# Kernel tuning notes

Hardware: AMD Instinct MI355X
Metric: run time of the kernel (lower is better)

Reference implementation:

```python
import jax, jax.numpy as jnp
import numpy as np

FEAT = 256
NUM_ATOMS = np.array([2048, 1536, 1024, 2048, 512, 1792, 1280, 2048], dtype=np.int32)
B = len(NUM_ATOMS)
N = int(NUM_ATOMS.sum())          # 12288 total atoms
MAXN = int(NUM_ATOMS.max())       # 2048
# Static segment bookkeeping (num_atoms is structural, not data)
_OFFSETS = np.concatenate([[0], np.cumsum(NUM_ATOMS)[:-1]])
SEG = np.repeat(np.arange(B), NUM_ATOMS)            # [N] graph id per atom
POS = np.arange(N) - _OFFSETS[SEG]                  # [N] position within graph
VALID = np.arange(MAXN)[None, :] < NUM_ATOMS[:, None]  # [B, MAXN] key mask


def setup_inputs() -> dict:
    key = jax.random.key(0)
    k1, k2 = jax.random.split(key)
    s = jax.random.normal(k1, (N, FEAT), jnp.float32)
    # dense: feat_dim -> 3*feat_dim, with bias
    W = jax.random.normal(k2, (FEAT, 3 * FEAT), jnp.float32) / np.float32(np.sqrt(FEAT))
    b = jnp.zeros((3 * FEAT,), jnp.float32)
    num_atoms = jnp.asarray(NUM_ATOMS)
    return {"s": s, "W": W, "b": b, "num_atoms": num_atoms}


def _pad(X):
    # scatter flat [N, FEAT] atoms into padded [B, MAXN, FEAT]
    return jnp.zeros((B, MAXN, FEAT), X.dtype).at[SEG, POS].set(X)


def reference(s, W, b, num_atoms):
    qkv = s @ W + b                          # [N, 3*FEAT]
    Q, K, V = jnp.split(qkv, 3, axis=-1)     # each [N, FEAT]
    Qp, Kp, Vp = _pad(Q), _pad(K), _pad(V)   # [B, MAXN, FEAT]
    scale = np.float32(1.0 / np.sqrt(FEAT))
    scores = jnp.einsum('bqd,bkd->bqk', Qp, Kp) * scale   # [B, MAXN, MAXN]
    scores = jnp.where(VALID[:, None, :], scores, -jnp.inf)  # mask padded keys
    att = jax.nn.softmax(scores, axis=-1)
    out = jnp.einsum('bqk,bkd->bqd', att, Vp)             # [B, MAXN, FEAT]
    return out[SEG, POS]                                   # back to flat [N, FEAT]
```

## Files before the change

kernel.cpp:

```cpp
#include <hip/hip_runtime.h>

typedef __attribute__((ext_vector_type(8))) short short8;
typedef __attribute__((ext_vector_type(4))) short s16x4;
typedef __attribute__((ext_vector_type(4))) float f32x4;

#define MFMA16(a,b,c) __builtin_amdgcn_mfma_f32_16x16x32_bf16((a),(b),(c),0,0,0)

__device__ __forceinline__ ushort f2bf(float f){ union{float f; unsigned u;} v; v.f=f; unsigned r=v.u + 0x7fffu + ((v.u>>16)&1u); return (ushort)(r>>16); }
__device__ __forceinline__ float bf2f(ushort u){ union{unsigned u; float f;} v; v.u = ((unsigned)u)<<16; return v.f; }

__global__ void __launch_bounds__(256) prep(const float* __restrict__ S,
    ushort* __restrict__ Sb, const float* __restrict__ W, ushort* __restrict__ Wt)
{
    __shared__ __align__(16) ushort tile[64*72];
    const int t = threadIdx.x;
    if (blockIdx.x < 1024){
        const int tid = blockIdx.x*256 + t;
#pragma unroll
        for (int r=0;r<3;r++){
            const int idx = tid + r*262144;
            f32x4 v = ((const f32x4*)S)[idx];
            s16x4 o;
            o[0]=(short)f2bf(v[0]); o[1]=(short)f2bf(v[1]);
            o[2]=(short)f2bf(v[2]); o[3]=(short)f2bf(v[3]);
            ((s16x4*)Sb)[idx] = o;
        }
    } else {
        const int i = blockIdx.x - 1024;
        const int r0 = (i&3)*64, c0 = (i>>2)*64;
        const int rr = t>>2, g = (t&3)*16;
        const float* sp = W + (size_t)(r0+rr)*768 + c0 + g;
#pragma unroll
        for (int j=0;j<16;j++) tile[(g+j)*72 + rr] = f2bf(sp[j]);
        __syncthreads();
        ushort* dp = Wt + (size_t)(c0+rr)*256 + r0 + g;
        *(short8*)dp     = *(const short8*)&tile[rr*72 + g];
        *(short8*)(dp+8) = *(const short8*)&tile[rr*72 + g + 8];
    }
}

__global__ void __launch_bounds__(256) qkv_gemm(const ushort* __restrict__ Sb,
    const ushort* __restrict__ Wt, const float* __restrict__ bias,
    ushort* __restrict__ Q, ushort* __restrict__ K, ushort* __restrict__ Vt)
{
    __shared__ __align__(16) ushort Bl[64*264];
    const int t = threadIdx.x, w = t>>6, l = t&63, lr = l&15, lq = l>>4;
    const int m0 = blockIdx.x*128, n0 = blockIdx.y*64;

    const ushort* ap = Sb + (size_t)(m0 + w*32 + lr)*256 + lq*8;
    short8 sa[2][8];
#pragma unroll
    for (int g=0;g<2;g++)
#pragma unroll
        for (int kc=0;kc<8;kc++)
            sa[g][kc] = *(const short8*)(ap + g*16*256 + kc*32);

#pragma unroll
    for (int s=0;s<8;s++){
        const int u = t + s*256, row = u>>5, c8 = u&31;
        *(short8*)&Bl[row*264 + c8*8] = *(const short8*)(Wt + (size_t)(n0+row)*256 + c8*8);
    }
    __syncthreads();

    if (n0 < 512){
        f32x4 acc[2][4];
#pragma unroll
        for (int a=0;a<2;a++)
#pragma unroll
            for (int b2=0;b2<4;b2++) acc[a][b2]=(f32x4){0.f,0.f,0.f,0.f};
#pragma unroll
        for (int kc=0;kc<8;kc++){
#pragma unroll
            for (int nt=0;nt<4;nt++){
                short8 bf = *(const short8*)&Bl[(nt*16+lr)*264 + lq*8 + kc*32];
                acc[0][nt] = MFMA16(sa[0][kc], bf, acc[0][nt]);
                acc[1][nt] = MFMA16(sa[1][kc], bf, acc[1][nt]);
            }
        }
        ushort* dst = (n0 < 256) ? Q : K;
        const int colbase = n0 & 255;
#pragma unroll
        for (int nt=0;nt<4;nt++){
            float bv = bias[n0 + nt*16 + lr];
#pragma unroll
            for (int mt=0;mt<2;mt++){
                const int row = m0 + w*32 + mt*16 + lq*4;
                ushort* o = dst + (size_t)row*256 + colbase + nt*16 + lr;
#pragma unroll
                for (int i=0;i<4;i++) o[(size_t)i*256] = f2bf(acc[mt][nt][i] + bv);
            }
        }
    } else {
        const int f0 = n0 - 512;
        f32x4 acc[4][2];
#pragma unroll
        for (int a=0;a<4;a++)
#pragma unroll
            for (int b2=0;b2<2;b2++) acc[a][b2]=(f32x4){0.f,0.f,0.f,0.f};
#pragma unroll
        for (int kc=0;kc<8;kc++){
#pragma unroll
            for (int ft=0;ft<4;ft++){
                short8 af = *(const short8*)&Bl[(ft*16+lr)*264 + lq*8 + kc*32];
                acc[ft][0] = MFMA16(af, sa[0][kc], acc[ft][0]);
                acc[ft][1] = MFMA16(af, sa[1][kc], acc[ft][1]);
            }
        }
#pragma unroll
        for (int ft=0;ft<4;ft++){
#pragma unroll
            for (int at=0;at<2;at++){
                ushort* o = Vt + (size_t)(f0 + ft*16 + lq*4)*12288 + m0 + w*32 + at*16 + lr;
#pragma unroll
                for (int i=0;i<4;i++){
                    float bv = bias[512 + f0 + ft*16 + lq*4 + i];
                    o[(size_t)i*12288] = f2bf(acc[ft][at][i] + bv);
                }
            }
        }
    }
}

template<int MODE>
__global__ void __launch_bounds__(256,2) attn_partial(const ushort* __restrict__ Qb,
    const ushort* __restrict__ Kb, const ushort* __restrict__ Vt,
    void* __restrict__ Optr, float* __restrict__ Lptr)
{
    __shared__ __align__(16) ushort Kl[32*264];
    __shared__ __align__(16) ushort Vl[256*40];
    const int t = threadIdx.x, w = t>>6, l = t&63, lr = l&15, lq = l>>4;

    const int offs[9] = {0,2048,3584,4608,6656,7168,8960,10240,12288};
    int bi = blockIdx.x, q0=0, kstart=0, kend=0, off=0, nbg=0, pbase=0, pb=0;
#pragma unroll
    for (int s=0;s<8;s++){
        const int nb = offs[s+1]-offs[s];
        const int tiles = nb>>7, pieces = (nb+511)>>9;
        const int items = tiles*pieces;
        if (bi >= 0 && bi < items){
            const int tile = bi / pieces, piece = bi - tile*pieces;
            q0 = offs[s] + tile*128;
            kstart = offs[s] + piece*512;
            kend = min(offs[s]+nb, kstart+512);
            off = offs[s]; nbg = nb; pbase = pb;
        }
        bi -= items;
        pb += nb*pieces;
    }
    const int nchunks = (kend - kstart) >> 5;
    const int pc = (kstart - off) >> 9;

    short8 qf[2][8];
#pragma unroll
    for (int g=0;g<2;g++){
        const ushort* qp = Qb + (size_t)(q0 + w*32 + g*16 + lr)*256 + lq*8;
#pragma unroll
        for (int kc=0;kc<8;kc++) qf[g][kc] = *(const short8*)(qp + kc*32);
    }
    f32x4 Oa[2][16];
#pragma unroll
    for (int g=0;g<2;g++)
#pragma unroll
        for (int ft=0;ft<16;ft++) Oa[g][ft] = (f32x4){0.f,0.f,0.f,0.f};
    float l_lane[2] = {0.f, 0.f};

    const int kr = t>>5, kcol = t&31;
    const ushort* kg0 = Kb + (size_t)(kstart + kr)*256 + kcol*8;
    const ushort* vg0 = Vt + (size_t)t*12288 + kstart;
    short8 kreg[4], vreg[4];
#pragma unroll
    for (int s=0;s<4;s++){
        kreg[s] = *(const short8*)(kg0 + (size_t)s*8*256);
        vreg[s] = *(const short8*)(vg0 + s*8);
    }

    const int i0 = 4*(lr + 32*(lq&1));
    const int i1 = i0 + 64;
    const bool hi = (lq >= 2);

    for (int ck=0; ck<nchunks; ck++){
#pragma unroll
        for (int s=0;s<4;s++)
            *(short8*)&Kl[(kr + s*8)*264 + kcol*8] = kreg[s];
#pragma unroll
        for (int s=0;s<4;s++)
            *(short8*)&Vl[t*40 + s*8] = vreg[s];
        if (ck+1 < nchunks){
            const ushort* kg = kg0 + (size_t)(ck+1)*32*256;
            const ushort* vg = vg0 + (ck+1)*32;
#pragma unroll
            for (int s=0;s<4;s++){
                kreg[s] = *(const short8*)(kg + (size_t)s*8*256);
                vreg[s] = *(const short8*)(vg + s*8);
            }
        }
        __syncthreads();

        f32x4 sc[2][2];
#pragma unroll
        for (int h=0;h<2;h++)
#pragma unroll
            for (int g=0;g<2;g++) sc[h][g] = (f32x4){0.f,0.f,0.f,0.f};
#pragma unroll
        for (int kc=0;kc<8;kc++){
            short8 b0 = *(const short8*)&Kl[ lr     *264 + kc*32 + lq*8];
            short8 b1 = *(const short8*)&Kl[(16+lr)*264 + kc*32 + lq*8];
#pragma unroll
            for (int g=0;g<2;g++){
                sc[0][g] = MFMA16(b0, qf[g][kc], sc[0][g]);
                sc[1][g] = MFMA16(b1, qf[g][kc], sc[1][g]);
            }
        }

        short8 pa[2];
#pragma unroll
        for (int g=0;g<2;g++){
            float p[8];
#pragma unroll
            for (int h=0;h<2;h++)
#pragma unroll
                for (int i=0;i<4;i++){
                    float v = exp2f(sc[h][g][i]*0.0901684284f);
                    p[h*4+i] = v;
                    l_lane[g] += v;
                }
            unsigned w0 = (unsigned)f2bf(p[0]) | ((unsigned)f2bf(p[1])<<16);
            unsigned w1 = (unsigned)f2bf(p[2]) | ((unsigned)f2bf(p[3])<<16);
            unsigned w2 = (unsigned)f2bf(p[4]) | ((unsigned)f2bf(p[5])<<16);
            unsigned w3 = (unsigned)f2bf(p[6]) | ((unsigned)f2bf(p[7])<<16);
            unsigned a0 = (unsigned)__builtin_amdgcn_ds_bpermute(i0, (int)w0);
            unsigned a2 = (unsigned)__builtin_amdgcn_ds_bpermute(i0, (int)w2);
            unsigned b1w= (unsigned)__builtin_amdgcn_ds_bpermute(i0, (int)w1);
            unsigned b3 = (unsigned)__builtin_amdgcn_ds_bpermute(i0, (int)w3);
            unsigned c0 = (unsigned)__builtin_amdgcn_ds_bpermute(i1, (int)w0);
            unsigned c2 = (unsigned)__builtin_amdgcn_ds_bpermute(i1, (int)w2);
            unsigned d1 = (unsigned)__builtin_amdgcn_ds_bpermute(i1, (int)w1);
            unsigned d3 = (unsigned)__builtin_amdgcn_ds_bpermute(i1, (int)w3);
            union { unsigned u[4]; short8 s8; } pk;
            pk.u[0] = hi ? a2 : a0;
            pk.u[1] = hi ? b3 : b1w;
            pk.u[2] = hi ? c2 : c0;
            pk.u[3] = hi ? d3 : d1;
            pa[g] = pk.s8;
        }

#pragma unroll
        for (int ft=0;ft<16;ft++){
            short8 vf = *(const short8*)&Vl[(ft*16+lr)*40 + lq*8];
            Oa[0][ft] = MFMA16(pa[0], vf, Oa[0][ft]);
            Oa[1][ft] = MFMA16(pa[1], vf, Oa[1][ft]);
        }
        __syncthreads();
    }

#pragma unroll
    for (int g=0;g<2;g++){
        float r = l_lane[g];
        r += __shfl_xor(r,16); r += __shfl_xor(r,32);
        l_lane[g] = r;
    }

    if constexpr (MODE == 0){
        ushort* Op = (ushort*)Optr;
        const int prow0 = pbase + pc*nbg + (q0 + w*32 - off);
#pragma unroll
        for (int g=0;g<2;g++)
#pragma unroll
            for (int i=0;i<4;i++){
                ushort* o = Op + (size_t)(prow0 + g*16 + lq*4 + i)*256 + lr;
#pragma unroll
                for (int ft=0;ft<16;ft++) o[ft*16] = f2bf(Oa[g][ft][i]);
            }
        if (l < 16){
            Lptr[prow0 + lr]      = l_lane[0];
            Lptr[prow0 + 16 + lr] = l_lane[1];
        }
    } else {
        float* out = (float*)Optr;
#pragma unroll
        for (int g=0;g<2;g++){
            float* op = out + (size_t)(q0 + w*32 + g*16 + lq*4)*256 + lr;
#pragma unroll
            for (int i=0;i<4;i++)
#pragma unroll
                for (int ft=0;ft<16;ft++)
                    atomicAdd(&op[(size_t)i*256 + ft*16], Oa[g][ft][i]);
        }
        if (l < 16){
            atomicAdd(&Lptr[q0 + w*32 + lr],      l_lane[0]);
            atomicAdd(&Lptr[q0 + w*32 + 16 + lr], l_lane[1]);
        }
    }
}

__global__ void __launch_bounds__(256) reduce_norm(const ushort* __restrict__ Opart,
    const float* __restrict__ Lpart, float* __restrict__ out, int PL)
{
    const int offs[9] = {0,2048,3584,4608,6656,7168,8960,10240,12288};
    const int t = threadIdx.x;
    const int row = blockIdx.x*8 + (t>>5);
    const int f = (t&31)*8;
    const int PIECE = 1 << PL;
    int pb = 0, nb = 0, S = 0, base = 0;
#pragma unroll
    for (int i=0;i<8;i++){
        const int nbi = offs[i+1]-offs[i];
        const int pieces = (nbi + PIECE-1) >> PL;
        if (row >= offs[i] && row < offs[i+1]){
            nb = nbi; S = pieces; base = pb + (row - offs[i]);
        }
        pb += nbi*pieces;
    }
    float acc[8] = {0.f,0.f,0.f,0.f,0.f,0.f,0.f,0.f};
    float L = 0.f;
    for (int p=0; p<S; p++){
        const size_t pr = (size_t)(base + p*nb);
        L += Lpart[pr];
        short8 v = *(const short8*)&Opart[pr*256 + f];
#pragma unroll
        for (int j=0;j<8;j++) acc[j] += bf2f((ushort)v[j]);
    }
    const float inv = 1.0f / L;
    f32x4 o0, o1;
#pragma unroll
    for (int j=0;j<4;j++){ o0[j] = acc[j]*inv; o1[j] = acc[4+j]*inv; }
    float* op = out + (size_t)row*256 + f;
    *(f32x4*)op     = o0;
    *(f32x4*)(op+4) = o1;
}

__global__ void __launch_bounds__(256) normalize_out(float* __restrict__ out,
    const float* __restrict__ lsum)
{
    const int row = blockIdx.x, t = threadIdx.x;
    const float inv = 1.0f / lsum[row];
    out[(size_t)row*256 + t] *= inv;
}

extern "C" void kernel_launch(void* const* d_in, const int* in_sizes, int n_in,
                              void* d_out, int out_size, void* d_ws, size_t ws_size,
                              hipStream_t stream)
{
    const float* S    = nullptr;
    const float* W    = nullptr;
    const float* bias = nullptr;
    for (int i = 0; i < n_in; i++){
        if      (in_sizes[i] == 3145728) S    = (const float*)d_in[i];
        else if (in_sizes[i] ==  196608) W    = (const float*)d_in[i];
        else if (in_sizes[i] ==     768) bias = (const float*)d_in[i];
    }
    if (!S)    S    = (const float*)d_in[0];
    if (!W)    W    = (const float*)d_in[1];
    if (!bias) bias = (const float*)d_in[2];

    float* out = (float*)d_out;

    ushort* ws  = (ushort*)d_ws;
    ushort* Wt  = ws;
    ushort* Qb  = Wt + 768*256;
    ushort* Kb  = Qb + 12288*256;
    ushort* Vtb = Kb + 12288*256;

    const size_t base_b  = ((size_t)768*256 + 3*(size_t)12288*256) * 2;
    const size_t need512 = base_b + (size_t)42752*512 + (size_t)42752*4;

    ushort* Sb = (ushort*)d_out;

    prep     <<<1072,        256, 0, stream>>>(S, Sb, W, Wt);
    qkv_gemm <<<dim3(96,12), 256, 0, stream>>>(Sb, Wt, bias, Qb, Kb, Vtb);

    if (ws_size >= need512){
        ushort* Opart = (ushort*)((char*)d_ws + base_b);
        float*  Lpart = (float*)((char*)d_ws + base_b + (size_t)42752*512);
        attn_partial<0><<<334, 256, 0, stream>>>(Qb, Kb, Vtb, (void*)Opart, Lpart);
        reduce_norm    <<<1536, 256, 0, stream>>>(Opart, Lpart, out, 9);
    } else {
        float* lsum = (float*)((char*)d_ws + base_b);
        (void)hipMemsetAsync(d_out, 0, (size_t)12288*256*4, stream);
        (void)hipMemsetAsync(lsum,  0, (size_t)12288*4,     stream);
        attn_partial<1><<<334, 256, 0, stream>>>(Qb, Kb, Vtb, (void*)out, lsum);
        normalize_out  <<<12288, 256, 0, stream>>>(out, lsum);
    }
}
```

Baseline: 158.7 us.

## Block the V-transpose layout per 32-key chunk and transpose PV MFMA output

Stores the transposed V as contiguous 32-key blocks of 256 features, so each attention chunk's V loads come from one contiguous 16KB region instead of 256 rows strided by 12288. It also swaps the MFMA operand order in the PV product so the accumulator holds transposed tiles. That lets partial outputs be written as packed 4-element vectors per row, and atomics hit consecutive addresses. Both the producer and consumer index math change, so they must stay consistent.

```diff
diff --git a/kernel.cpp b/kernel.cpp
--- a/kernel.cpp
+++ b/kernel.cpp
@@ -106,15 +106,16 @@
                 acc[ft][1] = MFMA16(af, sa[1][kc], acc[ft][1]);
             }
         }
+        ushort* vbase = Vt + (size_t)(blockIdx.x*4 + w)*8192;
 #pragma unroll
         for (int ft=0;ft<4;ft++){
 #pragma unroll
             for (int at=0;at<2;at++){
-                ushort* o = Vt + (size_t)(f0 + ft*16 + lq*4)*12288 + m0 + w*32 + at*16 + lr;
+                ushort* o = vbase + (f0 + ft*16 + lq*4)*32 + at*16 + lr;
 #pragma unroll
                 for (int i=0;i<4;i++){
                     float bv = bias[512 + f0 + ft*16 + lq*4 + i];
-                    o[(size_t)i*12288] = f2bf(acc[ft][at][i] + bv);
+                    o[i*32] = f2bf(acc[ft][at][i] + bv);
                 }
             }
         }
@@ -166,7 +167,7 @@
 
     const int kr = t>>5, kcol = t&31;
     const ushort* kg0 = Kb + (size_t)(kstart + kr)*256 + kcol*8;
-    const ushort* vg0 = Vt + (size_t)t*12288 + kstart;
+    const ushort* vg0 = Vt + (size_t)(kstart>>5)*8192 + t*32;
     short8 kreg[4], vreg[4];
 #pragma unroll
     for (int s=0;s<4;s++){
@@ -187,7 +188,7 @@
             *(short8*)&Vl[t*40 + s*8] = vreg[s];
         if (ck+1 < nchunks){
             const ushort* kg = kg0 + (size_t)(ck+1)*32*256;
-            const ushort* vg = vg0 + (ck+1)*32;
+            const ushort* vg = vg0 + (size_t)(ck+1)*8192;
 #pragma unroll
             for (int s=0;s<4;s++){
                 kreg[s] = *(const short8*)(kg + (size_t)s*8*256);
@@ -247,8 +248,8 @@
 #pragma unroll
         for (int ft=0;ft<16;ft++){
             short8 vf = *(const short8*)&Vl[(ft*16+lr)*40 + lq*8];
-            Oa[0][ft] = MFMA16(pa[0], vf, Oa[0][ft]);
-            Oa[1][ft] = MFMA16(pa[1], vf, Oa[1][ft]);
+            Oa[0][ft] = MFMA16(vf, pa[0], Oa[0][ft]);
+            Oa[1][ft] = MFMA16(vf, pa[1], Oa[1][ft]);
         }
         __syncthreads();
     }
@@ -264,13 +265,16 @@
         ushort* Op = (ushort*)Optr;
         const int prow0 = pbase + pc*nbg + (q0 + w*32 - off);
 #pragma unroll
-        for (int g=0;g<2;g++)
-#pragma unroll
-            for (int i=0;i<4;i++){
-                ushort* o = Op + (size_t)(prow0 + g*16 + lq*4 + i)*256 + lr;
-#pragma unroll
-                for (int ft=0;ft<16;ft++) o[ft*16] = f2bf(Oa[g][ft][i]);
-            }
+        for (int g=0;g<2;g++){
+            ushort* orow = Op + (size_t)(prow0 + g*16 + lr)*256 + lq*4;
+#pragma unroll
+            for (int ft=0;ft<16;ft++){
+                s16x4 pk;
+                pk[0]=(short)f2bf(Oa[g][ft][0]); pk[1]=(short)f2bf(Oa[g][ft][1]);
+                pk[2]=(short)f2bf(Oa[g][ft][2]); pk[3]=(short)f2bf(Oa[g][ft][3]);
+                *(s16x4*)(orow + ft*16) = pk;
+            }
+        }
         if (l < 16){
             Lptr[prow0 + lr]      = l_lane[0];
             Lptr[prow0 + 16 + lr] = l_lane[1];
@@ -279,12 +283,12 @@
         float* out = (float*)Optr;
 #pragma unroll
         for (int g=0;g<2;g++){
-            float* op = out + (size_t)(q0 + w*32 + g*16 + lq*4)*256 + lr;
-#pragma unroll
-            for (int i=0;i<4;i++)
-#pragma unroll
-                for (int ft=0;ft<16;ft++)
-                    atomicAdd(&op[(size_t)i*256 + ft*16], Oa[g][ft][i]);
+            float* op = out + (size_t)(q0 + w*32 + g*16 + lr)*256 + lq*4;
+#pragma unroll
+            for (int ft=0;ft<16;ft++)
+#pragma unroll
+                for (int i=0;i<4;i++)
+                    atomicAdd(&op[ft*16 + i], Oa[g][ft][i]);
         }
         if (l < 16){
             atomicAdd(&Lptr[q0 + w*32 + lr],      l_lane[0]);
```

New measurement: 163.7 us. 3.1% more time.
